# Optimization experiments

Hardware: AMD Instinct MI355X
Metric: run time of the kernel (lower is better)

## Reference

```python
import jax, jax.numpy as jnp
import numpy as np

B, S, D, H, HD, L, P = 32, 511, 512, 8, 64, 4, 501
PD = 32
FD = D - 2 * PD  # feature_proj output dim = hidden - 2*player_dim
DFF = 4 * D


def _pe(T, d):
    pos = jnp.arange(T, dtype=jnp.float32)[:, None]
    div = jnp.exp(jnp.arange(0, d, 2, dtype=jnp.float32) * (-np.log(10000.0) / d))
    pe = jnp.zeros((T, d), jnp.float32)
    pe = pe.at[:, 0::2].set(jnp.sin(pos * div))
    pe = pe.at[:, 1::2].set(jnp.cos(pos * div))
    return pe


def _ln(x, g, b, eps=1e-5):
    mu = x.mean(-1, keepdims=True)
    v = jnp.mean((x - mu) ** 2, -1, keepdims=True)
    return (x - mu) * jax.lax.rsqrt(v + eps) * g + b


def _forward(runs, wickets, overs, batters, bowlers, player_embed, Wf, bf,
             query_token, Wq, bq, Wk, bk, Wv, bv, Wo, bo,
             rec_s, bow_s, bat_s, W1, b1, W2, b2, g1, be1, g2, be2, Wout, bout):
    Bt, St = runs.shape
    T = St + 1
    # ball embedding: [B,S,3]@[3,FD] cat player embeds -> [B,S,D]
    feats = jnp.stack([runs, wickets, overs], -1) @ Wf + bf
    x = jnp.concatenate([feats, player_embed[batters], player_embed[bowlers]], -1)
    # append learned query token, add sinusoidal PE
    x = jnp.concatenate([x, jnp.broadcast_to(query_token, (Bt, 1, D))], 1)
    x = x + _pe(T, D)[None]
    # actor masks, padded with ones for the query row/col -> [B,T,T]
    sb = (bowlers[:, :, None] == bowlers[:, None, :]).astype(x.dtype)
    sm = (batters[:, :, None] == batters[:, None, :]).astype(x.dtype)
    row = jnp.ones((Bt, 1, St), x.dtype)
    col = jnp.ones((Bt, T, 1), x.dtype)
    sb = jnp.concatenate([jnp.concatenate([sb, row], 1), col], 2)
    sm = jnp.concatenate([jnp.concatenate([sm, row], 1), col], 2)
    causal = jnp.triu(jnp.ones((T, T), bool), 1)
    rec = jnp.arange(T, dtype=x.dtype) / T  # recency bias over key positions
    scale = 1.0 / np.float32(np.sqrt(HD))
    for l in range(L):
        q = (x @ Wq[l] + bq[l]).reshape(Bt, T, H, HD).transpose(0, 2, 1, 3)
        k = (x @ Wk[l] + bk[l]).reshape(Bt, T, H, HD).transpose(0, 2, 1, 3)
        v = (x @ Wv[l] + bv[l]).reshape(Bt, T, H, HD).transpose(0, 2, 1, 3)
        scores = jnp.einsum('bhqd,bhkd->bhqk', q, k) * scale
        # specialized head biases (num_heads >= 3)
        scores = scores.at[:, 0].add((rec_s[l] * rec)[None, None, :])
        scores = scores.at[:, 1].add(bow_s[l] * sb)
        scores = scores.at[:, 2].add(bat_s[l] * sm)
        scores = jnp.where(causal[None, None], -jnp.inf, scores)
        a = jax.nn.softmax(scores, axis=-1)
        o = jnp.einsum('bhqk,bhkd->bhqd', a, v).transpose(0, 2, 1, 3).reshape(Bt, T, D)
        x = _ln(x + o @ Wo[l] + bo[l], g1[l], be1[l])
        ff = jax.nn.gelu(x @ W1[l] + b1[l], approximate=False) @ W2[l] + b2[l]
        x = _ln(x + ff, g2[l], be2[l])
    return x[:, -1] @ Wout + bout  # [B, D]


def setup_inputs() -> dict:
    key = jax.random.key(0)
    ks = jax.random.split(key, 16)
    w = lambda k, sh: (0.02 * jax.random.normal(k, sh)).astype(jnp.float32)
    return {
        'runs': jax.random.uniform(ks[0], (B, S), jnp.float32),
        'wickets': jax.random.uniform(ks[1], (B, S), jnp.float32),
        'overs': jax.random.uniform(ks[2], (B, S), jnp.float32),
        'batters': jax.random.randint(ks[3], (B, S), 0, 500, jnp.int32),
        'bowlers': jax.random.randint(ks[4], (B, S), 0, 500, jnp.int32),
        'player_embed': w(ks[5], (P, PD)),
        'Wf': w(ks[6], (3, FD)), 'bf': jnp.zeros((FD,), jnp.float32),
        'query_token': jax.random.normal(ks[7], (1, 1, D), jnp.float32),
        'Wq': w(ks[8], (L, D, D)), 'bq': jnp.zeros((L, D), jnp.float32),
        'Wk': w(ks[9], (L, D, D)), 'bk': jnp.zeros((L, D), jnp.float32),
        'Wv': w(ks[10], (L, D, D)), 'bv': jnp.zeros((L, D), jnp.float32),
        'Wo': w(ks[11], (L, D, D)), 'bo': jnp.zeros((L, D), jnp.float32),
        'rec_s': jnp.full((L,), 0.5, jnp.float32),
        'bow_s': jnp.full((L,), 2.0, jnp.float32),
        'bat_s': jnp.full((L,), 2.0, jnp.float32),
        'W1': w(ks[12], (L, D, DFF)), 'b1': jnp.zeros((L, DFF), jnp.float32),
        'W2': w(ks[13], (L, DFF, D)), 'b2': jnp.zeros((L, D), jnp.float32),
        'g1': jnp.ones((L, D), jnp.float32), 'be1': jnp.zeros((L, D), jnp.float32),
        'g2': jnp.ones((L, D), jnp.float32), 'be2': jnp.zeros((L, D), jnp.float32),
        'Wout': w(ks[14], (D, D)), 'bout': jnp.zeros((D,), jnp.float32),
    }


def reference(runs, wickets, overs, batters, bowlers, player_embed, Wf, bf,
              query_token, Wq, bq, Wk, bk, Wv, bv, Wo, bo,
              rec_s, bow_s, bat_s, W1, b1, W2, b2, g1, be1, g2, be2, Wout, bout):
    return _forward(runs, wickets, overs, batters, bowlers, player_embed, Wf, bf,
                    query_token, Wq, bq, Wk, bk, Wv, bv, Wo, bo,
                    rec_s, bow_s, bat_s, W1, b1, W2, b2, g1, be1, g2, be2, Wout, bout)
```

## Files before the change

### kernel.cpp

```cpp
#include <hip/hip_runtime.h>
#include <math.h>

#define B_ 32
#define S_ 511
#define T_ 512
#define D_ 512
#define H_ 8
#define HD_ 64
#define L_ 4
#define P_ 501
#define PD_ 32
#define FD_ 448
#define DFF_ 2048

typedef __attribute__((ext_vector_type(8))) short bf16x8;
typedef __attribute__((ext_vector_type(4))) float f32x4;

#define GLDS16(gp, lp) __builtin_amdgcn_global_load_lds(                      \
    (const __attribute__((address_space(1))) void*)(gp),                      \
    (__attribute__((address_space(3))) void*)(lp), 16, 0, 0)

__device__ __forceinline__ unsigned short f2bf(float f) {
  union { float f; unsigned int u; } c; c.f = f;
  unsigned int r = c.u + 0x7FFFu + ((c.u >> 16) & 1u);
  return (unsigned short)(r >> 16);
}

__global__ __launch_bounds__(256) void wtrans_kernel(
    const float* __restrict__ in, unsigned short* __restrict__ out, int K, int N,
    size_t lstride, int nofs)
{
  __shared__ float t[64][65];
  const int l = blockIdx.z;
  in  += (size_t)l * K * N;
  out += (size_t)l * lstride + (size_t)nofs * K;
  const int k0 = blockIdx.x * 64, n0 = blockIdx.y * 64;
  const int tx = threadIdx.x & 63, ty = threadIdx.x >> 6;
#pragma unroll
  for (int i = 0; i < 16; ++i) {
    int r = ty + i * 4;
    t[r][tx] = in[(size_t)(k0 + r) * N + n0 + tx];
  }
  __syncthreads();
#pragma unroll
  for (int i = 0; i < 16; ++i) {
    int r = ty + i * 4;
    out[(size_t)(n0 + r) * K + k0 + tx] = f2bf(t[tx][r]);
  }
}

__global__ __launch_bounds__(256) void embed_kernel(
    const float* __restrict__ runs, const float* __restrict__ wickets,
    const float* __restrict__ overs, const int* __restrict__ batters,
    const int* __restrict__ bowlers, const float* __restrict__ pemb,
    const float* __restrict__ Wf, const float* __restrict__ bfv,
    const float* __restrict__ qtok, float* __restrict__ x,
    unsigned short* __restrict__ xb)
{
  size_t idx = (size_t)blockIdx.x * 256 + threadIdx.x;
  const size_t total = (size_t)B_ * T_ * D_;
  if (idx >= total) return;
  int d = (int)(idx % D_);
  int t = (int)((idx / D_) % T_);
  int b = (int)(idx / ((size_t)D_ * T_));
  float val;
  if (t < S_) {
    size_t st = (size_t)b * S_ + t;
    if (d < FD_) {
      val = runs[st] * Wf[d] + wickets[st] * Wf[FD_ + d] + overs[st] * Wf[2 * FD_ + d] + bfv[d];
    } else if (d < FD_ + PD_) {
      val = pemb[(size_t)batters[st] * PD_ + (d - FD_)];
    } else {
      val = pemb[(size_t)bowlers[st] * PD_ + (d - FD_ - PD_)];
    }
  } else {
    val = qtok[d];
  }
  float div = expf((float)(2 * (d >> 1)) * (-9.210340371976184f / (float)D_));
  float ang = (float)t * div;
  val += (d & 1) ? cosf(ang) : sinf(ang);
  x[idx] = val;
  xb[idx] = f2bf(val);
}

template<int ACT>
__global__ __launch_bounds__(256) void mfma_gemm(
    const unsigned short* __restrict__ A, const unsigned short* __restrict__ Bt,
    const float* __restrict__ bias, float* __restrict__ C,
    unsigned short* __restrict__ Cb, int N, int K, const float* __restrict__ bias2)
{
  __shared__ unsigned short As[2][128 * 32];
  __shared__ unsigned short Bs[2][128 * 32];
  __shared__ unsigned short Ts[ACT == 3 ? 128 * 136 : 1];
  const int tid = threadIdx.x;
  const int m0 = blockIdx.y * 128, n0 = blockIdx.x * 128;
  const int lane = tid & 63, w = tid >> 6;
  const int wr = w >> 1, wc = w & 1;
  const int lr = lane & 15, lg = lane >> 4;

  f32x4 acc[4][4] = {};

  const int srow = w * 16 + (lane >> 2);
  const int sc8 = (lane & 3) * 8;
  const unsigned short* gA0 = A + (size_t)(m0 + srow) * K + sc8;
  const unsigned short* gA1 = gA0 + (size_t)64 * K;
  const unsigned short* gB0 = Bt + (size_t)(n0 + srow) * K + sc8;
  const unsigned short* gB1 = gB0 + (size_t)64 * K;
  const int lofs0 = (w * 16) * 32;
  const int lofs1 = (64 + w * 16) * 32;

#define STAGE(buf, kk)                                                        \
  do {                                                                        \
    GLDS16(gA0 + (kk), &As[buf][lofs0]);                                      \
    GLDS16(gA1 + (kk), &As[buf][lofs1]);                                      \
    GLDS16(gB0 + (kk), &Bs[buf][lofs0]);                                      \
    GLDS16(gB1 + (kk), &Bs[buf][lofs1]);                                      \
  } while (0)

  STAGE(0, 0);
  __syncthreads();
  int cur = 0;
  for (int k0 = 0; k0 < K; k0 += 32) {
    if (k0 + 32 < K) STAGE(cur ^ 1, k0 + 32);
    bf16x8 af[4], bfr[4];
#pragma unroll
    for (int f = 0; f < 4; ++f) {
      af[f]  = *(const bf16x8*)&As[cur][(wr * 64 + f * 16 + lr) * 32 + lg * 8];
      bfr[f] = *(const bf16x8*)&Bs[cur][(wc * 64 + f * 16 + lr) * 32 + lg * 8];
    }
#pragma unroll
    for (int i = 0; i < 4; ++i)
#pragma unroll
      for (int j = 0; j < 4; ++j)
        acc[i][j] = __builtin_amdgcn_mfma_f32_16x16x32_bf16(af[i], bfr[j], acc[i][j], 0, 0, 0);
    __syncthreads();
    cur ^= 1;
  }
#undef STAGE

  const int crow0 = m0 + wr * 64 + lg * 4;
  const int ccol0 = n0 + wc * 64 + lr;
#pragma unroll
  for (int i = 0; i < 4; ++i) {
#pragma unroll
    for (int j = 0; j < 4; ++j) {
      const int col = ccol0 + j * 16;
      const float bcol = (ACT == 4) ? ((col < 512) ? bias[col] : bias2[col - 512])
                                    : bias[col];
#pragma unroll
      for (int r = 0; r < 4; ++r) {
        const int row = crow0 + i * 16 + r;
        float v = acc[i][j][r] + bcol;
        if (ACT == 1) {
          v = 0.5f * v * (1.0f + erff(v * 0.70710678118654752f));
          Cb[(size_t)row * N + col] = f2bf(v);
        } else if (ACT == 2 || ACT == 4) {
          Cb[(size_t)row * N + col] = f2bf(v);
        } else if (ACT == 3) {
          Ts[(wc * 64 + j * 16 + lr) * 136 + (wr * 64 + i * 16 + lg * 4 + r)] = f2bf(v);
        } else {
          C[(size_t)row * N + col] = v;
        }
      }
    }
  }
  if (ACT == 3) {
    __syncthreads();
    const int c = tid & 127, h2 = tid >> 7;
    const int hh = (n0 + c) >> 6, hd = (n0 + c) & 63;
    const int bb = m0 >> 9, t0 = (m0 & (T_ - 1)) + h2 * 64;
    unsigned short* dst = Cb + (((size_t)bb * H_ + hh) * HD_ + hd) * T_ + t0;
#pragma unroll
    for (int e = 0; e < 8; ++e)
      *(bf16x8*)(dst + e * 8) = *(const bf16x8*)&Ts[c * 136 + h2 * 64 + e * 8];
  }
}

__global__ __launch_bounds__(256) void flash_mfma_kernel(
    const unsigned short* __restrict__ qk, const unsigned short* __restrict__ vt,
    unsigned short* __restrict__ o,
    const int* __restrict__ batters, const int* __restrict__ bowlers,
    const float* __restrict__ rec_sp, const float* __restrict__ bow_sp,
    const float* __restrict__ bat_sp, int l)
{
  __shared__ unsigned short QPs[64 * 70];
  __shared__ unsigned short Ks[2][64 * 70];
  __shared__ unsigned short Vs[2][64 * 70];
  __shared__ int aq_s[64], ak_s[2][64];

  const int p = blockIdx.x, h = blockIdx.y, b = blockIdx.z;
  const int tid = threadIdx.x;
  const int w = tid >> 6, lane = tid & 63;
  const int c = lane & 15, g = lane >> 4;
  const int NT = T_ / 64;

  int mode = 0; float hs = 0.f;
  if (h == 0) { mode = 1; hs = rec_sp[l]; }
  else if (h == 1) { mode = 2; hs = bow_sp[l]; }
  else if (h == 2) { mode = 3; hs = bat_sp[l]; }
  const int* actors = (mode == 2) ? bowlers : batters;

  const int sr = tid >> 2, sch = (tid & 3) * 16;
  const unsigned short* qbase = qk + (size_t)b * T_ * 1024 + h * HD_;
  const unsigned short* kbase = qbase + 512;
  const unsigned short* vbase = vt + ((size_t)(b * H_ + h) * HD_ + sr) * T_;

  for (int ph = 0; ph < 2; ++ph) {
    const int qt = (ph == 0) ? p : (NT - 1 - p);
    const int q0 = qt * 64;
    __syncthreads();

    {
      const unsigned short* src = qbase + (size_t)(q0 + sr) * 1024 + sch;
      *(bf16x8*)&QPs[sr * 70 + sch]     = *(const bf16x8*)src;
      *(bf16x8*)&QPs[sr * 70 + sch + 8] = *(const bf16x8*)(src + 8);
      const unsigned short* ksrc = kbase + (size_t)sr * 1024 + sch;
      *(bf16x8*)&Ks[0][sr * 70 + sch]     = *(const bf16x8*)ksrc;
      *(bf16x8*)&Ks[0][sr * 70 + sch + 8] = *(const bf16x8*)(ksrc + 8);
      const unsigned short* vsrc = vbase + sch;
      *(bf16x8*)&Vs[0][sr * 70 + sch]     = *(const bf16x8*)vsrc;
      *(bf16x8*)&Vs[0][sr * 70 + sch + 8] = *(const bf16x8*)(vsrc + 8);
    }
    if (tid < 64) {
      int qg_ = q0 + tid;
      aq_s[tid] = (mode >= 2 && qg_ < S_) ? actors[(size_t)b * S_ + qg_] : -1;
      ak_s[0][tid] = (mode >= 2 && tid < S_) ? actors[(size_t)b * S_ + tid] : -1;
    }
    __syncthreads();

    bf16x8 af0 = *(const bf16x8*)&QPs[(w * 16 + c) * 70 + g * 8];
    bf16x8 af1 = *(const bf16x8*)&QPs[(w * 16 + c) * 70 + 32 + g * 8];
    int aq4[4];
#pragma unroll
    for (int r = 0; r < 4; ++r) aq4[r] = aq_s[w * 16 + 4 * g + r];

    float m_r[4] = {-INFINITY, -INFINITY, -INFINITY, -INFINITY};
    float l_r[4] = {0.f, 0.f, 0.f, 0.f};
    f32x4 o_acc[4] = {};
    int cur = 0;

    for (int kt = 0; kt <= qt; ++kt) {
      const int k0 = kt * 64;
      const bool has_next = kt < qt;
      bf16x8 kr0, kr1, vr0, vr1;
      int akn = -1;
      if (has_next) {
        const int k0n = k0 + 64;
        const unsigned short* ksrc = kbase + (size_t)(k0n + sr) * 1024 + sch;
        kr0 = *(const bf16x8*)ksrc;
        kr1 = *(const bf16x8*)(ksrc + 8);
        const unsigned short* vsrc = vbase + k0n + sch;
        vr0 = *(const bf16x8*)vsrc;
        vr1 = *(const bf16x8*)(vsrc + 8);
        if (tid < 64) {
          int kg_ = k0n + tid;
          akn = (mode >= 2 && kg_ < S_) ? actors[(size_t)b * S_ + kg_] : -1;
        }
      }

      if (q0 + w * 16 + 15 >= k0) {
        f32x4 s[4] = {};
#pragma unroll
        for (int f = 0; f < 4; ++f) {
          bf16x8 b0 = *(const bf16x8*)&Ks[cur][(f * 16 + c) * 70 + g * 8];
          bf16x8 b1 = *(const bf16x8*)&Ks[cur][(f * 16 + c) * 70 + 32 + g * 8];
          s[f] = __builtin_amdgcn_mfma_f32_16x16x32_bf16(af0, b0, s[f], 0, 0, 0);
          s[f] = __builtin_amdgcn_mfma_f32_16x16x32_bf16(af1, b1, s[f], 0, 0, 0);
        }
        int ak4[4];
#pragma unroll
        for (int f = 0; f < 4; ++f) ak4[f] = ak_s[cur][f * 16 + c];

        float sv[4][4];
#pragma unroll
        for (int f = 0; f < 4; ++f) {
          const int kg = k0 + f * 16 + c;
#pragma unroll
          for (int r = 0; r < 4; ++r) {
            const int qg = q0 + w * 16 + 4 * g + r;
            float val = s[f][r] * 0.125f;
            if (mode == 1) {
              val = fmaf(hs, (float)kg * (1.0f / (float)T_), val);
            } else if (mode >= 2) {
              float eq = (qg == S_ || kg == S_) ? 1.0f : ((aq4[r] == ak4[f]) ? 1.0f : 0.0f);
              val = fmaf(hs, eq, val);
            }
            if (kg > qg) val = -INFINITY;
            sv[f][r] = val;
          }
        }
        float cr[4];
#pragma unroll
        for (int r = 0; r < 4; ++r) {
          float pm = fmaxf(fmaxf(sv[0][r], sv[1][r]), fmaxf(sv[2][r], sv[3][r]));
          pm = fmaxf(pm, __shfl_xor(pm, 1));
          pm = fmaxf(pm, __shfl_xor(pm, 2));
          pm = fmaxf(pm, __shfl_xor(pm, 4));
          pm = fmaxf(pm, __shfl_xor(pm, 8));
          float m_new = fmaxf(m_r[r], pm);
          cr[r] = __expf(m_r[r] - m_new);
          m_r[r] = m_new;
        }
        float rs[4] = {0.f, 0.f, 0.f, 0.f};
#pragma unroll
        for (int f = 0; f < 4; ++f) {
#pragma unroll
          for (int r = 0; r < 4; ++r) {
            float pv = __expf(sv[f][r] - m_r[r]);
            rs[r] += pv;
            QPs[(w * 16 + 4 * g + r) * 70 + f * 16 + c] = f2bf(pv);
          }
        }
#pragma unroll
        for (int r = 0; r < 4; ++r) {
          float t = rs[r];
          t += __shfl_xor(t, 1);
          t += __shfl_xor(t, 2);
          t += __shfl_xor(t, 4);
          t += __shfl_xor(t, 8);
          l_r[r] = l_r[r] * cr[r] + t;
#pragma unroll
          for (int f = 0; f < 4; ++f) o_acc[f][r] *= cr[r];
        }
        bf16x8 pa0 = *(const bf16x8*)&QPs[(w * 16 + c) * 70 + g * 8];
        bf16x8 pa1 = *(const bf16x8*)&QPs[(w * 16 + c) * 70 + 32 + g * 8];
#pragma unroll
        for (int f = 0; f < 4; ++f) {
          bf16x8 v0 = *(const bf16x8*)&Vs[cur][(f * 16 + c) * 70 + g * 8];
          bf16x8 v1 = *(const bf16x8*)&Vs[cur][(f * 16 + c) * 70 + 32 + g * 8];
          o_acc[f] = __builtin_amdgcn_mfma_f32_16x16x32_bf16(pa0, v0, o_acc[f], 0, 0, 0);
          o_acc[f] = __builtin_amdgcn_mfma_f32_16x16x32_bf16(pa1, v1, o_acc[f], 0, 0, 0);
        }
      }

      if (has_next) {
        *(bf16x8*)&Ks[cur ^ 1][sr * 70 + sch]     = kr0;
        *(bf16x8*)&Ks[cur ^ 1][sr * 70 + sch + 8] = kr1;
        *(bf16x8*)&Vs[cur ^ 1][sr * 70 + sch]     = vr0;
        *(bf16x8*)&Vs[cur ^ 1][sr * 70 + sch + 8] = vr1;
        if (tid < 64) ak_s[cur ^ 1][tid] = akn;
        __syncthreads();
        cur ^= 1;
      }
    }

#pragma unroll
    for (int r = 0; r < 4; ++r) {
      const float inv = 1.0f / l_r[r];
      const int row = q0 + w * 16 + 4 * g + r;
#pragma unroll
      for (int f = 0; f < 4; ++f)
        o[((size_t)b * T_ + row) * D_ + h * HD_ + f * 16 + c] = f2bf(o_acc[f][r] * inv);
    }
  }
}

__global__ __launch_bounds__(256) void add_ln_kernel(
    float* __restrict__ x, const float* __restrict__ y,
    const float* __restrict__ g, const float* __restrict__ be,
    unsigned short* __restrict__ xb)
{
  int row = blockIdx.x;
  int tid = threadIdx.x;
  size_t base = (size_t)row * D_;
  float v0 = x[base + tid] + y[base + tid];
  float v1 = x[base + tid + 256] + y[base + tid + 256];
  float s = v0 + v1;
  float s2 = v0 * v0 + v1 * v1;
  __shared__ float redA[4], redB[4];
#pragma unroll
  for (int off = 32; off > 0; off >>= 1) {
    s  += __shfl_down(s, off);
    s2 += __shfl_down(s2, off);
  }
  if ((tid & 63) == 0) { redA[tid >> 6] = s; redB[tid >> 6] = s2; }
  __syncthreads();
  float st  = redA[0] + redA[1] + redA[2] + redA[3];
  float s2t = redB[0] + redB[1] + redB[2] + redB[3];
  float mu = st * (1.0f / (float)D_);
  float var = s2t * (1.0f / (float)D_) - mu * mu;
  float r = rsqrtf(var + 1e-5f);
  float o0 = (v0 - mu) * r * g[tid] + be[tid];
  float o1 = (v1 - mu) * r * g[tid + 256] + be[tid + 256];
  x[base + tid]        = o0;
  x[base + tid + 256]  = o1;
  xb[base + tid]       = f2bf(o0);
  xb[base + tid + 256] = f2bf(o1);
}

__global__ __launch_bounds__(256) void final_kernel(
    const float* __restrict__ x, const float* __restrict__ Wout,
    const float* __restrict__ bout, float* __restrict__ out)
{
  __shared__ float xs[D_];
  int b = blockIdx.x;
  int n = blockIdx.y * 256 + threadIdx.x;
  const float* xr = x + ((size_t)b * T_ + (T_ - 1)) * D_;
  xs[threadIdx.x] = xr[threadIdx.x];
  xs[threadIdx.x + 256] = xr[threadIdx.x + 256];
  __syncthreads();
  float acc = bout[n];
  for (int kk = 0; kk < D_; ++kk)
    acc = fmaf(xs[kk], Wout[(size_t)kk * D_ + n], acc);
  out[(size_t)b * D_ + n] = acc;
}

extern "C" void kernel_launch(void* const* d_in, const int* in_sizes, int n_in,
                              void* d_out, int out_size, void* d_ws, size_t ws_size,
                              hipStream_t stream)
{
  const float* runs    = (const float*)d_in[0];
  const float* wickets = (const float*)d_in[1];
  const float* overs   = (const float*)d_in[2];
  const int*   batters = (const int*)d_in[3];
  const int*   bowlers = (const int*)d_in[4];
  const float* pemb    = (const float*)d_in[5];
  const float* Wf      = (const float*)d_in[6];
  const float* bfv     = (const float*)d_in[7];
  const float* qtok    = (const float*)d_in[8];
  const float* Wq      = (const float*)d_in[9];
  const float* bq      = (const float*)d_in[10];
  const float* Wk      = (const float*)d_in[11];
  const float* bk      = (const float*)d_in[12];
  const float* Wv      = (const float*)d_in[13];
  const float* bv      = (const float*)d_in[14];
  const float* Wo      = (const float*)d_in[15];
  const float* bo      = (const float*)d_in[16];
  const float* rec_s   = (const float*)d_in[17];
  const float* bow_s   = (const float*)d_in[18];
  const float* bat_s   = (const float*)d_in[19];
  const float* W1      = (const float*)d_in[20];
  const float* b1      = (const float*)d_in[21];
  const float* W2      = (const float*)d_in[22];
  const float* b2      = (const float*)d_in[23];
  const float* g1      = (const float*)d_in[24];
  const float* be1     = (const float*)d_in[25];
  const float* g2      = (const float*)d_in[26];
  const float* be2     = (const float*)d_in[27];
  const float* Wout    = (const float*)d_in[28];
  const float* bout    = (const float*)d_in[29];

  float* ws = (float*)d_ws;
  const size_t n1 = (size_t)B_ * T_ * D_;
  float* x  = ws;
  float* yb = ws + n1;
  unsigned short* xb = (unsigned short*)(ws + 2 * n1);
  unsigned short* qkb = xb + n1;
  unsigned short* vt  = qkb + 2 * n1;
  unsigned short* ob  = vt + n1;
  unsigned short* wt  = ob + n1;
  unsigned short* hb  = qkb;

  const size_t qk_lstride = (size_t)1024 * 512;
  unsigned short* wqk = wt;
  unsigned short* wtv = wqk + (size_t)L_ * qk_lstride;
  unsigned short* wto = wtv + (size_t)L_ * D_ * D_;
  unsigned short* wt1 = wto + (size_t)L_ * D_ * D_;
  unsigned short* wt2 = wt1 + (size_t)L_ * D_ * DFF_;

  const int M = B_ * T_;
  dim3 blk(256);

  wtrans_kernel<<<dim3(8, 8, L_),  blk, 0, stream>>>(Wq, wqk, D_, D_, qk_lstride, 0);
  wtrans_kernel<<<dim3(8, 8, L_),  blk, 0, stream>>>(Wk, wqk, D_, D_, qk_lstride, 512);
  wtrans_kernel<<<dim3(8, 8, L_),  blk, 0, stream>>>(Wv, wtv, D_, D_, (size_t)D_ * D_, 0);
  wtrans_kernel<<<dim3(8, 8, L_),  blk, 0, stream>>>(Wo, wto, D_, D_, (size_t)D_ * D_, 0);
  wtrans_kernel<<<dim3(8, 32, L_), blk, 0, stream>>>(W1, wt1, D_, DFF_, (size_t)D_ * DFF_, 0);
  wtrans_kernel<<<dim3(32, 8, L_), blk, 0, stream>>>(W2, wt2, DFF_, D_, (size_t)DFF_ * D_, 0);

  {
    size_t total = (size_t)B_ * T_ * D_;
    int nb = (int)((total + 255) / 256);
    embed_kernel<<<nb, blk, 0, stream>>>(runs, wickets, overs, batters, bowlers,
                                         pemb, Wf, bfv, qtok, x, xb);
  }

  for (int l = 0; l < L_; ++l) {
    mfma_gemm<4><<<dim3(1024 / 128, M / 128), blk, 0, stream>>>(
        xb, wqk + (size_t)l * qk_lstride, bq + l * D_, nullptr, qkb, 1024, D_,
        bk + l * D_);
    mfma_gemm<3><<<dim3(D_ / 128, M / 128), blk, 0, stream>>>(
        xb, wtv + (size_t)l * D_ * D_, bv + l * D_, nullptr, vt, D_, D_, nullptr);

    flash_mfma_kernel<<<dim3(T_ / 128, H_, B_), blk, 0, stream>>>(
        qkb, vt, ob, batters, bowlers, rec_s, bow_s, bat_s, l);

    mfma_gemm<0><<<dim3(D_ / 128, M / 128), blk, 0, stream>>>(
        ob, wto + (size_t)l * D_ * D_, bo + l * D_, yb, nullptr, D_, D_, nullptr);
    add_ln_kernel<<<M, blk, 0, stream>>>(x, yb, g1 + l * D_, be1 + l * D_, xb);

    mfma_gemm<1><<<dim3(DFF_ / 128, M / 128), blk, 0, stream>>>(
        xb, wt1 + (size_t)l * D_ * DFF_, b1 + l * DFF_, nullptr, hb, DFF_, D_, nullptr);
    mfma_gemm<0><<<dim3(D_ / 128, M / 128), blk, 0, stream>>>(
        hb, wt2 + (size_t)l * DFF_ * D_, b2 + l * D_, yb, nullptr, D_, DFF_, nullptr);
    add_ln_kernel<<<M, blk, 0, stream>>>(x, yb, g2 + l * D_, be2 + l * D_, xb);
  }

  final_kernel<<<dim3(B_, D_ / 256), blk, 0, stream>>>(x, Wout, bout, (float*)d_out);
}
```

Before: 1.349 ms.

## Add 256x256-tile 512-thread GEMM kernel for QK, O, FFN projections

Introduces a new GEMM kernel with 256x256 output tiles, K-step 64, 8 waves and double-buffered global-to-LDS loads with explicit waitcnt and barriers. It is used for the fused QK, output, FFN1 and FFN2 projections, while the V-transpose GEMM stays on the old 128x128 kernel (whose unused epilogue branches are removed). Larger tiles raise data reuse per LDS load and halve the operand traffic. The cost is 128KB of LDS per block and a large accumulator footprint, which lowers occupancy. The grid also becomes much smaller (for example 2x64 blocks for N=512), which may underfill the CUs.

```diff
diff --git a/kernel.cpp b/kernel.cpp
--- a/kernel.cpp
+++ b/kernel.cpp
@@ -84,6 +84,102 @@
 }
 
 template<int ACT>
+__global__ __launch_bounds__(512) void mfma_gemm256(
+    const unsigned short* __restrict__ A, const unsigned short* __restrict__ Bt,
+    const float* __restrict__ bias, float* __restrict__ C,
+    unsigned short* __restrict__ Cb, int N, int K, const float* __restrict__ bias2)
+{
+  __shared__ unsigned short As[2][256 * 64];
+  __shared__ unsigned short Bs[2][256 * 64];
+  const int tid = threadIdx.x;
+  const int m0 = blockIdx.y * 256, n0 = blockIdx.x * 256;
+  const int lane = tid & 63, w = tid >> 6;
+  const int wr = w >> 2, wc = w & 3;
+  const int lr = lane & 15, lg = lane >> 4;
+
+  f32x4 acc[8][4] = {};
+
+  const unsigned short* gA = A + (size_t)m0 * K;
+  const unsigned short* gB = Bt + (size_t)n0 * K;
+
+#define STAGE256(buf, kt)                                                     \
+  do {                                                                        \
+    const int k0s = (kt) * 64;                                                \
+    _Pragma("unroll")                                                         \
+    for (int i = 0; i < 4; ++i) {                                             \
+      int s = i * 512 + tid;                                                  \
+      GLDS16(gA + (size_t)(s >> 3) * K + k0s + (s & 7) * 8, &As[buf][s * 8]); \
+    }                                                                         \
+    _Pragma("unroll")                                                         \
+    for (int i = 0; i < 4; ++i) {                                             \
+      int s = i * 512 + tid;                                                  \
+      GLDS16(gB + (size_t)(s >> 3) * K + k0s + (s & 7) * 8, &Bs[buf][s * 8]); \
+    }                                                                         \
+  } while (0)
+
+  const int NK = K / 64;
+  STAGE256(0, 0);
+  for (int kt = 0; kt < NK; ++kt) {
+    if (kt + 1 < NK) {
+      STAGE256((kt + 1) & 1, kt + 1);
+      asm volatile("s_waitcnt vmcnt(8)" ::: "memory");
+    } else {
+      asm volatile("s_waitcnt vmcnt(0)" ::: "memory");
+    }
+    __builtin_amdgcn_s_barrier();
+    __builtin_amdgcn_sched_barrier(0);
+    {
+      const unsigned short* Ab = &As[kt & 1][0];
+      const unsigned short* Bb = &Bs[kt & 1][0];
+      bf16x8 bfrag[4][2];
+#pragma unroll
+      for (int ni = 0; ni < 4; ++ni) {
+        bfrag[ni][0] = *(const bf16x8*)&Bb[(wc * 64 + ni * 16 + lr) * 64 + lg * 8];
+        bfrag[ni][1] = *(const bf16x8*)&Bb[(wc * 64 + ni * 16 + lr) * 64 + 32 + lg * 8];
+      }
+#pragma unroll
+      for (int mi = 0; mi < 8; ++mi) {
+        bf16x8 a0 = *(const bf16x8*)&Ab[(wr * 128 + mi * 16 + lr) * 64 + lg * 8];
+        bf16x8 a1 = *(const bf16x8*)&Ab[(wr * 128 + mi * 16 + lr) * 64 + 32 + lg * 8];
+#pragma unroll
+        for (int ni = 0; ni < 4; ++ni) {
+          acc[mi][ni] = __builtin_amdgcn_mfma_f32_16x16x32_bf16(a0, bfrag[ni][0], acc[mi][ni], 0, 0, 0);
+          acc[mi][ni] = __builtin_amdgcn_mfma_f32_16x16x32_bf16(a1, bfrag[ni][1], acc[mi][ni], 0, 0, 0);
+        }
+      }
+    }
+    __builtin_amdgcn_s_barrier();
+    __builtin_amdgcn_sched_barrier(0);
+  }
+#undef STAGE256
+
+  const int crow0 = m0 + wr * 128 + lg * 4;
+  const int ccol0 = n0 + wc * 64 + lr;
+#pragma unroll
+  for (int mi = 0; mi < 8; ++mi) {
+#pragma unroll
+    for (int ni = 0; ni < 4; ++ni) {
+      const int col = ccol0 + ni * 16;
+      const float bcol = (ACT == 4) ? ((col < 512) ? bias[col] : bias2[col - 512])
+                                    : bias[col];
+#pragma unroll
+      for (int r = 0; r < 4; ++r) {
+        const int row = crow0 + mi * 16 + r;
+        float v = acc[mi][ni][r] + bcol;
+        if (ACT == 1) {
+          v = 0.5f * v * (1.0f + erff(v * 0.70710678118654752f));
+          Cb[(size_t)row * N + col] = f2bf(v);
+        } else if (ACT == 4) {
+          Cb[(size_t)row * N + col] = f2bf(v);
+        } else {
+          C[(size_t)row * N + col] = v;
+        }
+      }
+    }
+  }
+}
+
+template<int ACT>
 __global__ __launch_bounds__(256) void mfma_gemm(
     const unsigned short* __restrict__ A, const unsigned short* __restrict__ Bt,
     const float* __restrict__ bias, float* __restrict__ C,
@@ -145,18 +241,12 @@
 #pragma unroll
     for (int j = 0; j < 4; ++j) {
       const int col = ccol0 + j * 16;
-      const float bcol = (ACT == 4) ? ((col < 512) ? bias[col] : bias2[col - 512])
-                                    : bias[col];
+      const float bcol = bias[col];
 #pragma unroll
       for (int r = 0; r < 4; ++r) {
         const int row = crow0 + i * 16 + r;
         float v = acc[i][j][r] + bcol;
-        if (ACT == 1) {
-          v = 0.5f * v * (1.0f + erff(v * 0.70710678118654752f));
-          Cb[(size_t)row * N + col] = f2bf(v);
-        } else if (ACT == 2 || ACT == 4) {
-          Cb[(size_t)row * N + col] = f2bf(v);
-        } else if (ACT == 3) {
+        if (ACT == 3) {
           Ts[(wc * 64 + j * 16 + lr) * 136 + (wr * 64 + i * 16 + lg * 4 + r)] = f2bf(v);
         } else {
           C[(size_t)row * N + col] = v;
@@ -460,6 +550,7 @@
 
   const int M = B_ * T_;
   dim3 blk(256);
+  dim3 blk512(512);
 
   wtrans_kernel<<<dim3(8, 8, L_),  blk, 0, stream>>>(Wq, wqk, D_, D_, qk_lstride, 0);
   wtrans_kernel<<<dim3(8, 8, L_),  blk, 0, stream>>>(Wk, wqk, D_, D_, qk_lstride, 512);
@@ -476,7 +567,7 @@
   }
 
   for (int l = 0; l < L_; ++l) {
-    mfma_gemm<4><<<dim3(1024 / 128, M / 128), blk, 0, stream>>>(
+    mfma_gemm256<4><<<dim3(1024 / 256, M / 256), blk512, 0, stream>>>(
         xb, wqk + (size_t)l * qk_lstride, bq + l * D_, nullptr, qkb, 1024, D_,
         bk + l * D_);
     mfma_gemm<3><<<dim3(D_ / 128, M / 128), blk, 0, stream>>>(
@@ -485,13 +576,13 @@
     flash_mfma_kernel<<<dim3(T_ / 128, H_, B_), blk, 0, stream>>>(
         qkb, vt, ob, batters, bowlers, rec_s, bow_s, bat_s, l);
 
-    mfma_gemm<0><<<dim3(D_ / 128, M / 128), blk, 0, stream>>>(
+    mfma_gemm256<0><<<dim3(D_ / 256, M / 256), blk512, 0, stream>>>(
         ob, wto + (size_t)l * D_ * D_, bo + l * D_, yb, nullptr, D_, D_, nullptr);
     add_ln_kernel<<<M, blk, 0, stream>>>(x, yb, g1 + l * D_, be1 + l * D_, xb);
 
-    mfma_gemm<1><<<dim3(DFF_ / 128, M / 128), blk, 0, stream>>>(
+    mfma_gemm256<1><<<dim3(DFF_ / 256, M / 256), blk512, 0, stream>>>(
         xb, wt1 + (size_t)l * D_ * DFF_, b1 + l * DFF_, nullptr, hb, DFF_, D_, nullptr);
-    mfma_gemm<0><<<dim3(D_ / 128, M / 128), blk, 0, stream>>>(
+    mfma_gemm256<0><<<dim3(D_ / 256, M / 256), blk512, 0, stream>>>(
         hb, wt2 + (size_t)l * DFF_ * D_, b2 + l * D_, yb, nullptr, D_, DFF_, nullptr);
     add_ln_kernel<<<M, blk, 0, stream>>>(x, yb, g2 + l * D_, be2 + l * D_, xb);
   }
```

Result: slower. 1.472 ms (+9.1%).
